# Optimization experiments

Hardware: AMD Instinct MI355X
Metric: run time of the kernel (lower is better)

The kernel has to match this reference:

```python
import jax, jax.numpy as jnp
import numpy as np

N = 100000          # number of road-network nodes
E = 640000          # number of directed edges (sparse adjacency nnz)
HID = 128           # hidden_dims = lane(16)+type(32)+length(16)+node(64)
N_LAYERS = 3        # hparams.baseline_gat_layer


def setup_inputs() -> dict:
    key = jax.random.key(0)
    ks = jax.random.split(key, 12)
    inp = {
        'node_feature': jax.random.randint(ks[0], (N,), 0, 100000),
        'type_feature': jax.random.randint(ks[1], (N,), 0, 20),
        'length_feature': jax.random.randint(ks[2], (N,), 0, 100),
        'lane_feature': jax.random.randint(ks[3], (N,), 0, 10),
        'adj_src': jax.random.randint(ks[4], (E,), 0, N),
        'adj_dst': jax.random.randint(ks[5], (E,), 0, N),
        'adj_val': jax.random.uniform(ks[6], (E,), dtype=jnp.float32),
        # learned parameters
        'node_emb': jax.random.normal(ks[7], (100000, 64), dtype=jnp.float32) * 0.02,
        'type_emb': jax.random.normal(ks[8], (20, 32), dtype=jnp.float32) * 0.02,
        'length_emb': jax.random.normal(ks[9], (100, 16), dtype=jnp.float32) * 0.02,
        'lane_emb': jax.random.normal(ks[10], (10, 16), dtype=jnp.float32) * 0.02,
        'W': jax.random.normal(ks[11], (HID, HID), dtype=jnp.float32) / np.sqrt(HID),
        'b': jnp.zeros((HID,), dtype=jnp.float32),
    }
    return inp


def spgcn_layer(x, W, b, adj_src, adj_dst, adj_val):
    # GCN layer: out = spmm(adj, x @ W) + b, adj given as COO edge list
    support = x @ W                                # [N, HID]
    msg = support[adj_src] * adj_val[:, None]      # gather + scale, [E, HID]
    agg = jax.ops.segment_sum(msg, adj_dst, num_segments=N)  # scatter-add
    return agg + b


def reference(node_feature, type_feature, length_feature, lane_feature,
              adj_src, adj_dst, adj_val,
              node_emb, type_emb, length_emb, lane_emb, W, b):
    # embedding lookups + concat: [lane, type, length, node] -> [N, HID]
    raw_feat = jnp.concatenate([
        lane_emb[lane_feature],
        type_emb[type_feature],
        length_emb[length_feature],
        node_emb[node_feature],
    ], axis=1)
    # repeated propagation with the SAME shared SPGCN layer weights
    for _ in range(N_LAYERS):
        raw_feat = spgcn_layer(raw_feat, W, b, adj_src, adj_dst, adj_val)
    return raw_feat
```

## Files before the change

kernel.cpp:

```cpp
#include <hip/hip_runtime.h>
#include <hip/hip_bf16.h>

typedef __hip_bfloat16 bf16;
typedef unsigned short ushort_t;
typedef __attribute__((ext_vector_type(8))) short short8;
typedef __attribute__((ext_vector_type(4))) float f32x4;

#define NN 100000
#define NE 640000
#define HD 128
#define NB 391
#define EMB_U 6250
#define PREP_U 64
#define CNT_U 391
#define PH0_U (EMB_U + PREP_U + CNT_U)
#define HIST_U 2500
#define GEMM_U 782
#define AGG_U 6250
#define D_U 391
#define LDA 136


__device__ __forceinline__ float bf2f(ushort_t u) {
    unsigned v = (unsigned)u << 16;
    return __builtin_bit_cast(float, v);
}
__device__ __forceinline__ ushort_t f2bf(float f) {
    bf16 h = __float2bfloat16(f);
    return *(ushort_t*)&h;
}

struct P {
    const int *nodef, *typef, *lenf, *lanef, *adj_src, *adj_dst;
    const float *adj_val, *node_emb, *type_emb, *len_emb, *lane_emb, *W, *bias;
    ushort_t *Xa, *Xb, *Wt, *w2t, *w3t;
    float *bw, *bw2, *d, *d2;
    int *cnt, *offs, *pos, *bsum;
    int2 *epack;
    float *outf;
};


__global__ __launch_bounds__(256) void phase0_k(P p) {
    const int v = blockIdx.x;
    const int tid = threadIdx.x;
    if (v < EMB_U) {
        const int idx = v * 256 + tid;
        const int i = idx >> 4;
        const int c = (idx & 15) * 8;
        const float* tbl; size_t base;
        if (c < 16)      { tbl = p.lane_emb; base = (size_t)p.lanef[i] * 16 + c; }
        else if (c < 48) { tbl = p.type_emb; base = (size_t)p.typef[i] * 32 + (c - 16); }
        else if (c < 64) { tbl = p.len_emb;  base = (size_t)p.lenf[i]  * 16 + (c - 48); }
        else             { tbl = p.node_emb; base = (size_t)p.nodef[i] * 64 + (c - 64); }
        const float4 f0 = *(const float4*)(tbl + base);
        const float4 f1 = *(const float4*)(tbl + base + 4);
        ushort_t u8[8] = { f2bf(f0.x), f2bf(f0.y), f2bf(f0.z), f2bf(f0.w),
                           f2bf(f1.x), f2bf(f1.y), f2bf(f1.z), f2bf(f1.w) };
        *(uint4*)(p.Xa + (size_t)i * HD + c) = *(uint4*)u8;
    } else if (v < EMB_U + PREP_U) {
        const int idx = (v - EMB_U) * 256 + tid;
        const int n = idx >> 7, k = idx & 127;
        p.Wt[idx] = f2bf(p.W[(size_t)k * HD + n]);
    } else {
        const int idx = (v - EMB_U - PREP_U) * 256 + tid;
        if (idx < NN) p.cnt[idx] = 0;
    }
}

__global__ __launch_bounds__(256) void histw_k(P p) {
    const int tid = threadIdx.x;
    if (blockIdx.x < HIST_U) {
        const int e = blockIdx.x * 256 + tid;
        atomicAdd(&p.cnt[p.adj_dst[e]], 1);
        return;
    }
    __shared__ ushort_t WtL[HD * HD];
    __shared__ float bwS[HD];
    for (int i = tid; i < HD * HD / 8; i += 256)
        *(uint4*)&WtL[i * 8] = *(const uint4*)&p.Wt[i * 8];
    __syncthreads();

    const int w = tid >> 6;
    const int ln = tid & 15;
    const int quad = (tid >> 4) & 3;
    const int koff = quad * 8;
    const f32x4 zero = {0.f, 0.f, 0.f, 0.f};

    short8 bfrg[2][4];
#pragma unroll
    for (int nt = 0; nt < 2; ++nt)
#pragma unroll
        for (int kc = 0; kc < 4; ++kc)
            bfrg[nt][kc] = *(const short8*)&WtL[(w * 32 + nt * 16 + ln) * HD + kc * 32 + koff];

#pragma unroll
    for (int mt = 0; mt < 8; ++mt) {
        const int m = mt * 16 + ln;
        short8 afrg[4];
#pragma unroll
        for (int kc = 0; kc < 4; ++kc) {
            ushort_t a[8];
#pragma unroll
            for (int j = 0; j < 8; ++j)
                a[j] = WtL[(kc * 32 + koff + j) * HD + m];
            afrg[kc] = *(short8*)a;
        }
        f32x4 acc[2] = {zero, zero};
#pragma unroll
        for (int nt = 0; nt < 2; ++nt)
#pragma unroll
            for (int kc = 0; kc < 4; ++kc)
                acc[nt] = __builtin_amdgcn_mfma_f32_16x16x32_bf16(
                        afrg[kc], bfrg[nt][kc], acc[nt], 0, 0, 0);
#pragma unroll
        for (int nt = 0; nt < 2; ++nt)
#pragma unroll
            for (int reg = 0; reg < 4; ++reg) {
                const int col = w * 32 + nt * 16 + ln;
                const int row = mt * 16 + quad * 4 + reg;
                p.w2t[col * HD + row] = f2bf(acc[nt][reg]);
            }
    }
    __syncthreads();

#pragma unroll
    for (int mt = 0; mt < 8; ++mt) {
        const int m = mt * 16 + ln;
        short8 afrg[4];
#pragma unroll
        for (int kc = 0; kc < 4; ++kc) {
            ushort_t a[8];
#pragma unroll
            for (int j = 0; j < 8; ++j)
                a[j] = p.w2t[(kc * 32 + koff + j) * HD + m];
            afrg[kc] = *(short8*)a;
        }
        f32x4 acc[2] = {zero, zero};
#pragma unroll
        for (int nt = 0; nt < 2; ++nt)
#pragma unroll
            for (int kc = 0; kc < 4; ++kc)
                acc[nt] = __builtin_amdgcn_mfma_f32_16x16x32_bf16(
                        afrg[kc], bfrg[nt][kc], acc[nt], 0, 0, 0);
#pragma unroll
        for (int nt = 0; nt < 2; ++nt)
#pragma unroll
            for (int reg = 0; reg < 4; ++reg) {
                const int col = w * 32 + nt * 16 + ln;
                const int row = mt * 16 + quad * 4 + reg;
                p.w3t[col * HD + row] = f2bf(acc[nt][reg]);
            }
    }
    __syncthreads();

    if (tid < HD) {
        float s = 0.f;
        for (int k = 0; k < HD; ++k) s += p.bias[k] * bf2f(WtL[tid * HD + k]);
        bwS[tid] = s;
        p.bw[tid] = s;
    }
    __syncthreads();
    if (tid < HD) {
        float s = 0.f;
        for (int k = 0; k < HD; ++k) s += bwS[k] * bf2f(WtL[tid * HD + k]);
        p.bw2[tid] = s;
    }
}


__global__ __launch_bounds__(256) void scan1_k(P p) {
    __shared__ int s[256];
    const int tid = threadIdx.x;
    const int idx = blockIdx.x * 256 + tid;
    s[tid] = (idx < NN) ? p.cnt[idx] : 0;
    __syncthreads();
    for (int o = 128; o; o >>= 1) {
        if (tid < o) s[tid] += s[tid + o];
        __syncthreads();
    }
    if (tid == 0) p.bsum[blockIdx.x] = s[0];
}

__global__ __launch_bounds__(256) void scan3_k(P p) {
    __shared__ int s[256];
    const int b = blockIdx.x;
    const int tid = threadIdx.x;
    int acc = 0;
    for (int i = tid; i < b; i += 256) acc += p.bsum[i];
    s[tid] = acc;
    __syncthreads();
    for (int o = 128; o; o >>= 1) {
        if (tid < o) s[tid] += s[tid + o];
        __syncthreads();
    }
    const int boffv = s[0];
    __syncthreads();
    const int idx = b * 256 + tid;
    int v = (idx < NN) ? p.cnt[idx] : 0;
    s[tid] = v;
    __syncthreads();
    for (int o = 1; o < 256; o <<= 1) {
        int x = (tid >= o) ? s[tid - o] : 0;
        __syncthreads();
        s[tid] += x;
        __syncthreads();
    }
    const int excl = s[tid] - v + boffv;
    if (idx <= NN) {
        p.offs[idx] = excl;
        if (idx < NN) p.pos[idx] = excl;
    }
}

__global__ __launch_bounds__(256) void position_k(P p) {
    const int e = blockIdx.x * 256 + threadIdx.x;
    const int d = p.adj_dst[e];
    const int slot = atomicAdd(&p.pos[d], 1);
    int2 pk;
    pk.x = p.adj_src[e];
    pk.y = __float_as_int(p.adj_val[e]);
    p.epack[slot] = pk;
}

__global__ __launch_bounds__(256) void agg_k(P p, const ushort_t* __restrict__ Xin,
                                             ushort_t* __restrict__ Xout, int aux) {
    if (blockIdx.x >= AGG_U) {
        const int node = (blockIdx.x - AGG_U) * 256 + threadIdx.x;
        if (node < NN) {
            const int lo = p.offs[node], hi = p.offs[node + 1];
            float s = 0.f;
            if (aux == 1) {
                for (int j = lo; j < hi; ++j) s += __int_as_float(p.epack[j].y);
                p.d[node] = s;
            } else {
                for (int j = lo; j < hi; ++j) {
                    const int2 e = p.epack[j];
                    s += __int_as_float(e.y) * p.d[e.x];
                }
                p.d2[node] = s;
            }
        }
        return;
    }
    const int node = blockIdx.x * 16 + (threadIdx.x >> 4);
    const int lane = threadIdx.x & 15;
    const int c = lane * 8;
    const int lo = p.offs[node];
    const int hi = p.offs[node + 1];
    float a0[8], a1[8], a2[8], a3[8];
#pragma unroll
    for (int k = 0; k < 8; ++k) { a0[k] = a1[k] = a2[k] = a3[k] = 0.f; }
    int j = lo;
    for (; j + 3 < hi; j += 4) {
        const int2 e0 = p.epack[j], e1 = p.epack[j + 1];
        const int2 e2 = p.epack[j + 2], e3 = p.epack[j + 3];
        const short8 u0 = *(const short8*)(Xin + (size_t)e0.x * HD + c);
        const short8 u1 = *(const short8*)(Xin + (size_t)e1.x * HD + c);
        const short8 u2 = *(const short8*)(Xin + (size_t)e2.x * HD + c);
        const short8 u3 = *(const short8*)(Xin + (size_t)e3.x * HD + c);
        const float v0 = __int_as_float(e0.y), v1 = __int_as_float(e1.y);
        const float v2 = __int_as_float(e2.y), v3 = __int_as_float(e3.y);
#pragma unroll
        for (int k = 0; k < 8; ++k) {
            a0[k] += bf2f((ushort_t)u0[k]) * v0;
            a1[k] += bf2f((ushort_t)u1[k]) * v1;
            a2[k] += bf2f((ushort_t)u2[k]) * v2;
            a3[k] += bf2f((ushort_t)u3[k]) * v3;
        }
    }
    for (; j < hi; ++j) {
        const int2 e0 = p.epack[j];
        const float v0 = __int_as_float(e0.y);
        const short8 u0 = *(const short8*)(Xin + (size_t)e0.x * HD + c);
#pragma unroll
        for (int k = 0; k < 8; ++k) a0[k] += bf2f((ushort_t)u0[k]) * v0;
    }
    ushort_t u8[8];
#pragma unroll
    for (int k = 0; k < 8; ++k) u8[k] = f2bf((a0[k] + a1[k]) + (a2[k] + a3[k]));
    *(uint4*)(Xout + (size_t)node * HD + c) = *(uint4*)u8;
}

__global__ __launch_bounds__(256) void gemmf_k(P p, const ushort_t* __restrict__ X2) {
    __shared__ ushort_t Xs[128 * LDA];
    const int tid = threadIdx.x;
    const int row0 = blockIdx.x * 128;

    {
        const int g = tid >> 4;
        const int lane = tid & 15;
        const int c = lane * 8;
        for (int mi = 0; mi < 8; ++mi) {
            const int m = g * 8 + mi;
            const int gm = row0 + m;
            float a0[8], a1[8], a2[8], a3[8];
#pragma unroll
            for (int k = 0; k < 8; ++k) { a0[k] = a1[k] = a2[k] = a3[k] = 0.f; }
            if (gm < NN) {
                const int lo = p.offs[gm];
                const int hi = p.offs[gm + 1];
                int j = lo;
                for (; j + 3 < hi; j += 4) {
                    const int2 e0 = p.epack[j], e1 = p.epack[j + 1];
                    const int2 e2 = p.epack[j + 2], e3 = p.epack[j + 3];
                    const short8 u0 = *(const short8*)(X2 + (size_t)e0.x * HD + c);
                    const short8 u1 = *(const short8*)(X2 + (size_t)e1.x * HD + c);
                    const short8 u2 = *(const short8*)(X2 + (size_t)e2.x * HD + c);
                    const short8 u3 = *(const short8*)(X2 + (size_t)e3.x * HD + c);
                    const float v0 = __int_as_float(e0.y), v1 = __int_as_float(e1.y);
                    const float v2 = __int_as_float(e2.y), v3 = __int_as_float(e3.y);
#pragma unroll
                    for (int k = 0; k < 8; ++k) {
                        a0[k] += bf2f((ushort_t)u0[k]) * v0;
                        a1[k] += bf2f((ushort_t)u1[k]) * v1;
                        a2[k] += bf2f((ushort_t)u2[k]) * v2;
                        a3[k] += bf2f((ushort_t)u3[k]) * v3;
                    }
                }
                for (; j < hi; ++j) {
                    const int2 e0 = p.epack[j];
                    const float v0 = __int_as_float(e0.y);
                    const short8 u0 = *(const short8*)(X2 + (size_t)e0.x * HD + c);
#pragma unroll
                    for (int k = 0; k < 8; ++k) a0[k] += bf2f((ushort_t)u0[k]) * v0;
                }
            }
            ushort_t u8[8];
#pragma unroll
            for (int k = 0; k < 8; ++k) u8[k] = f2bf((a0[k] + a1[k]) + (a2[k] + a3[k]));
            *(uint4*)&Xs[m * LDA + c] = *(uint4*)u8;
        }
    }

    const int w = tid >> 6;
    const int ln = tid & 15;
    const int quad = (tid >> 4) & 3;
    const int koff = quad * 8;
    const int col0 = w * 32 + ln;
    const int col1 = col0 + 16;

    short8 bfrg[2][4];
#pragma unroll
    for (int nt = 0; nt < 2; ++nt)
#pragma unroll
        for (int kc = 0; kc < 4; ++kc)
            bfrg[nt][kc] = *(const short8*)&p.w3t[(size_t)(w * 32 + nt * 16 + ln) * HD + kc * 32 + koff];

    const float bwc0 = p.bw[col0],  bwc1 = p.bw[col1];
    const float bw2c0 = p.bw2[col0], bw2c1 = p.bw2[col1];
    const float bc0 = p.bias[col0], bc1 = p.bias[col1];

    __syncthreads();

    const f32x4 zero = {0.f, 0.f, 0.f, 0.f};
#pragma unroll
    for (int mt = 0; mt < 8; ++mt) {
        short8 afrg[4];
#pragma unroll
        for (int kc = 0; kc < 4; ++kc)
            afrg[kc] = *(const short8*)&Xs[(mt * 16 + ln) * LDA + kc * 32 + koff];
        f32x4 acc[2] = {zero, zero};
#pragma unroll
        for (int nt = 0; nt < 2; ++nt)
#pragma unroll
            for (int kc = 0; kc < 4; ++kc)
                acc[nt] = __builtin_amdgcn_mfma_f32_16x16x32_bf16(
                        afrg[kc], bfrg[nt][kc], acc[nt], 0, 0, 0);
#pragma unroll
        for (int reg = 0; reg < 4; ++reg) {
            const int gm = row0 + mt * 16 + quad * 4 + reg;
            if (gm < NN) {
                const float dg = p.d[gm], d2g = p.d2[gm];
                p.outf[(size_t)gm * HD + col0] = acc[0][reg] + d2g * bw2c0 + dg * bwc0 + bc0;
                p.outf[(size_t)gm * HD + col1] = acc[1][reg] + d2g * bw2c1 + dg * bwc1 + bc1;
            }
        }
    }
}

extern "C" void kernel_launch(void* const* d_in, const int* in_sizes, int n_in,
                              void* d_out, int out_size, void* d_ws, size_t ws_size,
                              hipStream_t stream) {
    P p;
    p.nodef    = (const int*)d_in[0];
    p.typef    = (const int*)d_in[1];
    p.lenf     = (const int*)d_in[2];
    p.lanef    = (const int*)d_in[3];
    p.adj_src  = (const int*)d_in[4];
    p.adj_dst  = (const int*)d_in[5];
    p.adj_val  = (const float*)d_in[6];
    p.node_emb = (const float*)d_in[7];
    p.type_emb = (const float*)d_in[8];
    p.len_emb  = (const float*)d_in[9];
    p.lane_emb = (const float*)d_in[10];
    p.W        = (const float*)d_in[11];
    p.bias     = (const float*)d_in[12];
    p.outf     = (float*)d_out;

    const size_t xbytes = (size_t)NN * HD * 2;
    char* wp = (char*)d_ws;
    p.Xa    = (ushort_t*)wp; wp += xbytes;
    p.Xb    = (ushort_t*)wp; wp += xbytes;
    p.cnt   = (int*)wp;      wp += (size_t)NN * 4;
    p.offs  = (int*)wp;      wp += 400016;
    p.pos   = (int*)wp;      wp += (size_t)NN * 4;
    p.epack = (int2*)wp;     wp += (size_t)NE * 8;
    p.Wt    = (ushort_t*)wp; wp += 32768;
    p.w2t   = (ushort_t*)wp; wp += 32768;
    p.w3t   = (ushort_t*)wp; wp += 32768;
    p.bw    = (float*)wp;    wp += 512;
    p.bw2   = (float*)wp;    wp += 512;
    p.d     = (float*)wp;    wp += (size_t)NN * 4;
    p.d2    = (float*)wp;    wp += (size_t)NN * 4;
    p.bsum  = (int*)wp;      wp += 1600;

    phase0_k<<<PH0_U, 256, 0, stream>>>(p);
    histw_k<<<HIST_U + 1, 256, 0, stream>>>(p);
    scan1_k<<<NB, 256, 0, stream>>>(p);
    scan3_k<<<NB, 256, 0, stream>>>(p);
    position_k<<<HIST_U, 256, 0, stream>>>(p);
    agg_k<<<AGG_U + D_U, 256, 0, stream>>>(p, p.Xa, p.Xb, 1);
    agg_k<<<AGG_U + D_U, 256, 0, stream>>>(p, p.Xb, p.Xa, 2);
    gemmf_k<<<GEMM_U, 256, 0, stream>>>(p, p.Xa);
}
```

Baseline: 314.1 us.

## Record histogram slots to drop second atomic pass and overlap embedding with histogram

The histogram kernel now stores the atomicAdd return value per edge as a slot index. The position kernel then computes each edge's CSR location as offs[dst]+slot without a second round of atomics. The embedding gather moves into the same launch as the histogram and W-prep block, so those phases run concurrently, while the cnt zeroing and W transpose move to a small earlier kernel. This adds a 640K-int slots buffer that must be written and read, but removes one set of contended atomics and lets the histogram overlap with the embedding work.

```diff
diff --git a/kernel.cpp b/kernel.cpp
--- a/kernel.cpp
+++ b/kernel.cpp
@@ -13,7 +13,6 @@
 #define EMB_U 6250
 #define PREP_U 64
 #define CNT_U 391
-#define PH0_U (EMB_U + PREP_U + CNT_U)
 #define HIST_U 2500
 #define GEMM_U 782
 #define AGG_U 6250
@@ -35,17 +34,29 @@
     const float *adj_val, *node_emb, *type_emb, *len_emb, *lane_emb, *W, *bias;
     ushort_t *Xa, *Xb, *Wt, *w2t, *w3t;
     float *bw, *bw2, *d, *d2;
-    int *cnt, *offs, *pos, *bsum;
+    int *cnt, *offs, *slots, *bsum;
     int2 *epack;
     float *outf;
 };
 
 
-__global__ __launch_bounds__(256) void phase0_k(P p) {
+__global__ __launch_bounds__(256) void prep_k(P p) {
     const int v = blockIdx.x;
     const int tid = threadIdx.x;
-    if (v < EMB_U) {
+    if (v < CNT_U) {
         const int idx = v * 256 + tid;
+        if (idx < NN) p.cnt[idx] = 0;
+    } else {
+        const int idx = (v - CNT_U) * 256 + tid;
+        const int n = idx >> 7, k = idx & 127;
+        p.Wt[idx] = f2bf(p.W[(size_t)k * HD + n]);
+    }
+}
+
+__global__ __launch_bounds__(256) void ehist_k(P p) {
+    const int tid = threadIdx.x;
+    if (blockIdx.x >= 1 + HIST_U) {
+        const int idx = (blockIdx.x - 1 - HIST_U) * 256 + tid;
         const int i = idx >> 4;
         const int c = (idx & 15) * 8;
         const float* tbl; size_t base;
@@ -58,21 +69,11 @@
         ushort_t u8[8] = { f2bf(f0.x), f2bf(f0.y), f2bf(f0.z), f2bf(f0.w),
                            f2bf(f1.x), f2bf(f1.y), f2bf(f1.z), f2bf(f1.w) };
         *(uint4*)(p.Xa + (size_t)i * HD + c) = *(uint4*)u8;
-    } else if (v < EMB_U + PREP_U) {
-        const int idx = (v - EMB_U) * 256 + tid;
-        const int n = idx >> 7, k = idx & 127;
-        p.Wt[idx] = f2bf(p.W[(size_t)k * HD + n]);
-    } else {
-        const int idx = (v - EMB_U - PREP_U) * 256 + tid;
-        if (idx < NN) p.cnt[idx] = 0;
-    }
-}
-
-__global__ __launch_bounds__(256) void histw_k(P p) {
-    const int tid = threadIdx.x;
-    if (blockIdx.x < HIST_U) {
-        const int e = blockIdx.x * 256 + tid;
-        atomicAdd(&p.cnt[p.adj_dst[e]], 1);
+        return;
+    }
+    if (blockIdx.x >= 1) {
+        const int e = (blockIdx.x - 1) * 256 + tid;
+        p.slots[e] = atomicAdd(&p.cnt[p.adj_dst[e]], 1);
         return;
     }
     __shared__ ushort_t WtL[HD * HD];
@@ -207,20 +208,16 @@
         __syncthreads();
     }
     const int excl = s[tid] - v + boffv;
-    if (idx <= NN) {
-        p.offs[idx] = excl;
-        if (idx < NN) p.pos[idx] = excl;
-    }
-}
-
-__global__ __launch_bounds__(256) void position_k(P p) {
+    if (idx <= NN) p.offs[idx] = excl;
+}
+
+__global__ __launch_bounds__(256) void pos_k(P p) {
     const int e = blockIdx.x * 256 + threadIdx.x;
-    const int d = p.adj_dst[e];
-    const int slot = atomicAdd(&p.pos[d], 1);
+    const int dst = p.adj_dst[e];
     int2 pk;
     pk.x = p.adj_src[e];
     pk.y = __float_as_int(p.adj_val[e]);
-    p.epack[slot] = pk;
+    p.epack[p.offs[dst] + p.slots[e]] = pk;
 }
 
 __global__ __launch_bounds__(256) void agg_k(P p, const ushort_t* __restrict__ Xin,
@@ -404,7 +401,7 @@
     p.Xb    = (ushort_t*)wp; wp += xbytes;
     p.cnt   = (int*)wp;      wp += (size_t)NN * 4;
     p.offs  = (int*)wp;      wp += 400016;
-    p.pos   = (int*)wp;      wp += (size_t)NN * 4;
+    p.slots = (int*)wp;      wp += (size_t)NE * 4;
     p.epack = (int2*)wp;     wp += (size_t)NE * 8;
     p.Wt    = (ushort_t*)wp; wp += 32768;
     p.w2t   = (ushort_t*)wp; wp += 32768;
@@ -415,11 +412,11 @@
     p.d2    = (float*)wp;    wp += (size_t)NN * 4;
     p.bsum  = (int*)wp;      wp += 1600;
 
-    phase0_k<<<PH0_U, 256, 0, stream>>>(p);
-    histw_k<<<HIST_U + 1, 256, 0, stream>>>(p);
+    prep_k<<<CNT_U + PREP_U, 256, 0, stream>>>(p);
+    ehist_k<<<1 + HIST_U + EMB_U, 256, 0, stream>>>(p);
     scan1_k<<<NB, 256, 0, stream>>>(p);
     scan3_k<<<NB, 256, 0, stream>>>(p);
-    position_k<<<HIST_U, 256, 0, stream>>>(p);
+    pos_k<<<HIST_U, 256, 0, stream>>>(p);
     agg_k<<<AGG_U + D_U, 256, 0, stream>>>(p, p.Xa, p.Xb, 1);
     agg_k<<<AGG_U + D_U, 256, 0, stream>>>(p, p.Xb, p.Xa, 2);
     gemmf_k<<<GEMM_U, 256, 0, stream>>>(p, p.Xa);
```

After: 292.6 us. 1.07x faster.
